# Optimization experiments

Measured on AMD Instinct MI355X. Metric: run time of the kernel, lower is better.

## Reference

```python
import jax, jax.numpy as jnp
import numpy as np

B, T, C = 2, 2048, 1024
H = 16
HS = C // H
EPS = 1e-5


def layernorm(x, g, b):
    mu = jnp.mean(x, axis=-1, keepdims=True)
    var = jnp.var(x, axis=-1, keepdims=True)
    return (x - mu) * jax.lax.rsqrt(var + EPS) * g + b


def setup_inputs() -> dict:
    key = jax.random.key(0)
    ks = jax.random.split(key, 12)
    s_in = 1.0 / np.sqrt(C)
    s_ff = 1.0 / np.sqrt(4 * C)
    return {
        "x": jax.random.normal(ks[0], (B, T, C), jnp.float32),
        "Wq": jax.random.normal(ks[1], (H, C, HS), jnp.float32) * s_in,
        "Wk": jax.random.normal(ks[2], (H, C, HS), jnp.float32) * s_in,
        "Wv": jax.random.normal(ks[3], (H, C, HS), jnp.float32) * s_in,
        "Wo": jax.random.normal(ks[4], (C, C), jnp.float32) * s_in,
        "bo": jnp.zeros((C,), jnp.float32),
        "W1": jax.random.normal(ks[5], (C, 4 * C), jnp.float32) * s_in,
        "b1": jnp.zeros((4 * C,), jnp.float32),
        "W2": jax.random.normal(ks[6], (4 * C, C), jnp.float32) * s_ff,
        "b2": jnp.zeros((C,), jnp.float32),
        "g1": jnp.ones((C,), jnp.float32),
        "be1": jnp.zeros((C,), jnp.float32),
        "g2": jnp.ones((C,), jnp.float32),
        "be2": jnp.zeros((C,), jnp.float32),
    }


def reference(x, Wq, Wk, Wv, Wo, bo, W1, b1, W2, b2, g1, be1, g2, be2):
    # x: [B,T,C]. Dropout is identity (eval mode).
    x = layernorm(x, g1, be1)
    # --- multi-head causal self-attention (per-source: scale by C**-0.5, NOT head_size) ---
    q = jnp.einsum("btc,hcd->bhtd", x, Wq)
    k = jnp.einsum("btc,hcd->bhtd", x, Wk)
    v = jnp.einsum("btc,hcd->bhtd", x, Wv)
    scores = jnp.einsum("bhtd,bhsd->bhts", q, k) * (C ** -0.5)  # [B,H,T,T]
    causal = jnp.tril(jnp.ones((T, T), bool))
    scores = jnp.where(causal, scores, -jnp.inf)
    wei = jax.nn.softmax(scores, axis=-1)
    attn = jnp.einsum("bhts,bhsd->bhtd", wei, v)
    attn = attn.transpose(0, 2, 1, 3).reshape(B, T, C)  # concat heads on last dim
    sa = attn @ Wo + bo
    x = x + sa
    # --- MLP with second pre-op LayerNorm ---
    x = layernorm(x, g2, be2)
    h = jax.nn.relu(x @ W1 + b1)
    x = x + (h @ W2 + b2)
    return x
```

## Files before the change

### kernel.cpp

```cpp
#include <hip/hip_runtime.h>
#include <hip/hip_bf16.h>
#include <math.h>

#define B_ 2
#define T_ 2048
#define C_ 1024
#define H_ 16
#define HS_ 64
#define N_ROWS (B_*T_)
#define MB (1024*1024)

typedef __attribute__((ext_vector_type(8))) short bf16x8;
typedef __attribute__((ext_vector_type(8))) unsigned short u16x8;
typedef __attribute__((ext_vector_type(4))) float floatx4;

static __device__ __forceinline__ unsigned short f2bf(float f) {
  union { float f; unsigned u; } v; v.f = f;
  unsigned r = v.u + 0x7fff + ((v.u >> 16) & 1);
  return (unsigned short)(r >> 16);
}
static __device__ __forceinline__ float bf2f(unsigned short s) {
  union { unsigned u; float f; } v; v.u = ((unsigned)s) << 16;
  return v.f;
}

__global__ __launch_bounds__(256) void ln_kernel(
    const float* __restrict__ x, const float* __restrict__ g,
    const float* __restrict__ b, unsigned short* __restrict__ outb)
{
  const int row = blockIdx.x;
  const int tid = threadIdx.x;
  const float* xr = x + (size_t)row * C_;
  float4 xv = *reinterpret_cast<const float4*>(xr + tid * 4);
  float s  = xv.x + xv.y + xv.z + xv.w;
  float ss = xv.x*xv.x + xv.y*xv.y + xv.z*xv.z + xv.w*xv.w;
  #pragma unroll
  for (int off = 32; off > 0; off >>= 1) {
    s  += __shfl_down(s, off, 64);
    ss += __shfl_down(ss, off, 64);
  }
  __shared__ float rs[4], rss[4];
  __shared__ float smu, srstd;
  if ((tid & 63) == 0) { rs[tid >> 6] = s; rss[tid >> 6] = ss; }
  __syncthreads();
  if (tid == 0) {
    float S  = rs[0] + rs[1] + rs[2] + rs[3];
    float SS = rss[0] + rss[1] + rss[2] + rss[3];
    float mu  = S * (1.0f / C_);
    float var = SS * (1.0f / C_) - mu * mu;
    smu = mu; srstd = rsqrtf(var + 1e-5f);
  }
  __syncthreads();
  const float mu = smu, rstd = srstd;
  float4 gv = *reinterpret_cast<const float4*>(g + tid * 4);
  float4 bv = *reinterpret_cast<const float4*>(b + tid * 4);
  union { unsigned long long ll; unsigned short s[4]; } o;
  o.s[0] = f2bf((xv.x - mu) * rstd * gv.x + bv.x);
  o.s[1] = f2bf((xv.y - mu) * rstd * gv.y + bv.y);
  o.s[2] = f2bf((xv.z - mu) * rstd * gv.z + bv.z);
  o.s[3] = f2bf((xv.w - mu) * rstd * gv.w + bv.w);
  *reinterpret_cast<unsigned long long*>(outb + (size_t)row * C_ + tid * 4) = o.ll;
}

__global__ __launch_bounds__(256) void transpose_cast(
    const float* __restrict__ in, unsigned short* __restrict__ out, int R, int Cc)
{
  __shared__ float tile[32][33];
  const int bz = blockIdx.z;
  in  += (size_t)bz * R * Cc;
  out += (size_t)bz * R * Cc;
  const int tx = threadIdx.x & 31;
  const int ty = threadIdx.x >> 5;
  const int c0 = blockIdx.x * 32, r0 = blockIdx.y * 32;
  #pragma unroll
  for (int j = 0; j < 4; ++j)
    tile[ty + j*8][tx] = in[(size_t)(r0 + ty + j*8) * Cc + c0 + tx];
  __syncthreads();
  #pragma unroll
  for (int j = 0; j < 4; ++j)
    out[(size_t)(c0 + ty + j*8) * R + r0 + tx] = f2bf(tile[tx][ty + j*8]);
}

__global__ __launch_bounds__(256) void transpose_cast_qkv(
    const float* __restrict__ Wq, const float* __restrict__ Wk,
    const float* __restrict__ Wv, unsigned short* __restrict__ out)
{
  __shared__ float tile[32][33];
  const int z = blockIdx.z;
  const int which = z >> 4, h = z & 15;
  const float* in = (which == 0 ? Wq : which == 1 ? Wk : Wv) + (size_t)h * C_ * HS_;
  unsigned short* dst = out + (size_t)z * C_ * HS_;
  const int tx = threadIdx.x & 31;
  const int ty = threadIdx.x >> 5;
  const int c0 = blockIdx.x * 32, r0 = blockIdx.y * 32;
  #pragma unroll
  for (int j = 0; j < 4; ++j)
    tile[ty + j*8][tx] = in[(size_t)(r0 + ty + j*8) * HS_ + c0 + tx];
  __syncthreads();
  #pragma unroll
  for (int j = 0; j < 4; ++j)
    dst[(size_t)(c0 + ty + j*8) * C_ + r0 + tx] = f2bf(tile[tx][ty + j*8]);
}

template<int TNB, bool OUTBF16, bool RELU, bool HASB, bool HASRES>
__global__ __launch_bounds__(256) void gemm_bf16(
    const unsigned short* __restrict__ A,
    const unsigned short* __restrict__ Bt,
    const float* __restrict__ bias,
    const unsigned short* __restrict__ res,
    void* __restrict__ Cout,
    int M, int N, int K)
{
  constexpr int NT = TNB / 32;
  constexpr int WN = TNB / 2;
  __shared__ unsigned short As[2][128 * 32];
  __shared__ unsigned short Bs[2][TNB * 32];
  const int tid  = threadIdx.x;
  const int lane = tid & 63;
  const int wave = tid >> 6;
  const int wm = wave & 1, wn = wave >> 1;
  const int m0 = blockIdx.x * 128, n0 = blockIdx.y * TNB;

  const int lrow = lane >> 2;
  const int lcol = (lane & 3) * 8;
  const int fr = lane & 15;
  const int fq = lane >> 4;

  floatx4 acc[4][NT] = {};

  const unsigned short* Aw = A  + (size_t)m0 * K;
  const unsigned short* Bw = Bt + (size_t)n0 * K;

  for (int k0 = 0; k0 < K; k0 += 64) {
    __syncthreads();
    #pragma unroll
    for (int half = 0; half < 2; ++half) {
      #pragma unroll
      for (int i = 0; i < 2; ++i) {
        const int rbase = i * 64 + wave * 16;
        const unsigned short* gp =
            Aw + (size_t)(rbase + lrow) * K + k0 + half * 32 + lcol;
        __builtin_amdgcn_global_load_lds(
            (const __attribute__((address_space(1))) void*)gp,
            (__attribute__((address_space(3))) void*)(As[half] + rbase * 32),
            16, 0, 0);
      }
      #pragma unroll
      for (int i = 0; i < TNB / 64; ++i) {
        const int rbase = i * 64 + wave * 16;
        const unsigned short* gp =
            Bw + (size_t)(rbase + lrow) * K + k0 + half * 32 + lcol;
        __builtin_amdgcn_global_load_lds(
            (const __attribute__((address_space(1))) void*)gp,
            (__attribute__((address_space(3))) void*)(Bs[half] + rbase * 32),
            16, 0, 0);
      }
    }
    __syncthreads();

    #pragma unroll
    for (int half = 0; half < 2; ++half) {
      bf16x8 af[4], bfr[NT];
      #pragma unroll
      for (int t = 0; t < 4; ++t)
        af[t]  = *reinterpret_cast<const bf16x8*>(
            As[half] + (wm*64 + t*16 + fr)*32 + fq*8);
      #pragma unroll
      for (int t = 0; t < NT; ++t)
        bfr[t] = *reinterpret_cast<const bf16x8*>(
            Bs[half] + (wn*WN + t*16 + fr)*32 + fq*8);
      #pragma unroll
      for (int mt = 0; mt < 4; ++mt)
        #pragma unroll
        for (int nt = 0; nt < NT; ++nt)
          acc[mt][nt] = __builtin_amdgcn_mfma_f32_16x16x32_bf16(
              af[mt], bfr[nt], acc[mt][nt], 0, 0, 0);
    }
  }

  #pragma unroll
  for (int nt = 0; nt < NT; ++nt) {
    const int col = n0 + wn*WN + nt*16 + fr;
    const float bv = HASB ? bias[col] : 0.0f;
    #pragma unroll
    for (int mt = 0; mt < 4; ++mt) {
      #pragma unroll
      for (int r = 0; r < 4; ++r) {
        const int row = m0 + wm*64 + mt*16 + fq*4 + r;
        float v = acc[mt][nt][r] + bv;
        if (RELU) v = v > 0.0f ? v : 0.0f;
        if (HASRES) v += bf2f(res[(size_t)row * N + col]);
        if (OUTBF16) ((unsigned short*)Cout)[(size_t)row * N + col] = f2bf(v);
        else         ((float*)Cout)[(size_t)row * N + col] = v;
      }
    }
  }
}

template<int TNB, int SPLITS>
__global__ __launch_bounds__(256) void gemm_splitk(
    const unsigned short* __restrict__ A,
    const unsigned short* __restrict__ Bt,
    unsigned short* __restrict__ Cpart,
    int M, int N, int Kfull)
{
  constexpr int NT = TNB / 32;
  constexpr int WN = TNB / 2;
  __shared__ unsigned short As[2][128 * 32];
  __shared__ unsigned short Bs[2][TNB * 32];
  const int tid  = threadIdx.x;
  const int lane = tid & 63;
  const int wave = tid >> 6;
  const int wm = wave & 1, wn = wave >> 1;
  const int m0 = blockIdx.x * 128, n0 = blockIdx.y * TNB;
  const int z  = blockIdx.z;
  const int Kh = Kfull / SPLITS;

  const int lrow = lane >> 2;
  const int lcol = (lane & 3) * 8;
  const int fr = lane & 15;
  const int fq = lane >> 4;

  floatx4 acc[4][NT] = {};

  const unsigned short* Aw = A  + (size_t)m0 * Kfull + (size_t)z * Kh;
  const unsigned short* Bw = Bt + (size_t)n0 * Kfull + (size_t)z * Kh;
  unsigned short* Cw = Cpart + (size_t)z * M * N;

  for (int k0 = 0; k0 < Kh; k0 += 64) {
    __syncthreads();
    #pragma unroll
    for (int half = 0; half < 2; ++half) {
      #pragma unroll
      for (int i = 0; i < 2; ++i) {
        const int rbase = i * 64 + wave * 16;
        const unsigned short* gp =
            Aw + (size_t)(rbase + lrow) * Kfull + k0 + half * 32 + lcol;
        __builtin_amdgcn_global_load_lds(
            (const __attribute__((address_space(1))) void*)gp,
            (__attribute__((address_space(3))) void*)(As[half] + rbase * 32),
            16, 0, 0);
      }
      #pragma unroll
      for (int i = 0; i < TNB / 64; ++i) {
        const int rbase = i * 64 + wave * 16;
        const unsigned short* gp =
            Bw + (size_t)(rbase + lrow) * Kfull + k0 + half * 32 + lcol;
        __builtin_amdgcn_global_load_lds(
            (const __attribute__((address_space(1))) void*)gp,
            (__attribute__((address_space(3))) void*)(Bs[half] + rbase * 32),
            16, 0, 0);
      }
    }
    __syncthreads();

    #pragma unroll
    for (int half = 0; half < 2; ++half) {
      bf16x8 af[4], bfr[NT];
      #pragma unroll
      for (int t = 0; t < 4; ++t)
        af[t]  = *reinterpret_cast<const bf16x8*>(
            As[half] + (wm*64 + t*16 + fr)*32 + fq*8);
      #pragma unroll
      for (int t = 0; t < NT; ++t)
        bfr[t] = *reinterpret_cast<const bf16x8*>(
            Bs[half] + (wn*WN + t*16 + fr)*32 + fq*8);
      #pragma unroll
      for (int mt = 0; mt < 4; ++mt)
        #pragma unroll
        for (int nt = 0; nt < NT; ++nt)
          acc[mt][nt] = __builtin_amdgcn_mfma_f32_16x16x32_bf16(
              af[mt], bfr[nt], acc[mt][nt], 0, 0, 0);
    }
  }

  #pragma unroll
  for (int nt = 0; nt < NT; ++nt) {
    const int col = n0 + wn*WN + nt*16 + fr;
    #pragma unroll
    for (int mt = 0; mt < 4; ++mt)
      #pragma unroll
      for (int r = 0; r < 4; ++r) {
        const int row = m0 + wm*64 + mt*16 + fq*4 + r;
        Cw[(size_t)row * N + col] = f2bf(acc[mt][nt][r]);
      }
  }
}

template<int SPLITS>
__global__ __launch_bounds__(256) void splitk_reduce(
    const unsigned short* __restrict__ p,
    const float* __restrict__ bias, const unsigned short* __restrict__ res,
    float* __restrict__ out)
{
  const size_t i = ((size_t)blockIdx.x * 256 + threadIdx.x) * 4;
  const size_t MN = (size_t)N_ROWS * C_;
  float4 bv = *reinterpret_cast<const float4*>(bias + (i & (size_t)(C_ - 1)));
  float acc[4] = {bv.x, bv.y, bv.z, bv.w};
  {
    const unsigned short* rp = res + i;
    #pragma unroll
    for (int j = 0; j < 4; ++j) acc[j] += bf2f(rp[j]);
  }
  #pragma unroll
  for (int z = 0; z < SPLITS; ++z) {
    const unsigned short* pp = p + (size_t)z * MN + i;
    #pragma unroll
    for (int j = 0; j < 4; ++j) acc[j] += bf2f(pp[j]);
  }
  float4 o; o.x = acc[0]; o.y = acc[1]; o.z = acc[2]; o.w = acc[3];
  *reinterpret_cast<float4*>(out + i) = o;
}

__global__ __launch_bounds__(256) void v_transpose(
    const unsigned short* __restrict__ qkv, unsigned short* __restrict__ vt)
{
  __shared__ __align__(16) unsigned short sT[64][72];
  const int st = blockIdx.x;
  const int bh = blockIdx.y;
  const int b = bh >> 4, h = bh & 15;
  const int t = threadIdx.x;
  const int r = t >> 2, c0 = (t & 3) * 16;
  const unsigned short* src =
      qkv + (size_t)(b * T_ + st * 64 + r) * 3072 + 2048 + h * 64 + c0;
  *(u16x8*)&sT[r][c0]     = *(const u16x8*)src;
  *(u16x8*)&sT[r][c0 + 8] = *(const u16x8*)(src + 8);
  __syncthreads();
  const int d = t >> 2, sc = (t & 3) * 16;
  unsigned short v[16];
  #pragma unroll
  for (int j = 0; j < 16; ++j) v[j] = sT[sc + j][d];
  unsigned short* dst = vt + ((size_t)bh * 64 + d) * (size_t)T_ + st * 64 + sc;
  *(uint4*)dst       = *(uint4*)&v[0];
  *(uint4*)(dst + 8) = *(uint4*)&v[8];
}

__global__ __launch_bounds__(256, 4) void attn_mfma(
    const unsigned short* __restrict__ qkv,
    const unsigned short* __restrict__ vt,
    unsigned short* __restrict__ out)
{
  const int bh = blockIdx.x;
  const int qt = (int)(gridDim.y - 1) - (int)blockIdx.y;
  const int b = bh >> 4, h = bh & 15;
  const int tid = threadIdx.x;
  const int w = tid >> 6;
  const int lane = tid & 63;
  const int l15 = lane & 15, fq = lane >> 4;
  const int t0 = qt * 64;
  const int q_row = t0 + w * 16 + l15;

  __shared__ __align__(16) unsigned short sK [64][72];
  __shared__ __align__(16) unsigned short sVt[64][72];
  __shared__ __align__(16) unsigned short sP [64][72];

  bf16x8 aq[2];
  {
    const unsigned short* qp = qkv + (size_t)(b*T_ + q_row)*3072 + h*HS_ + fq*8;
    aq[0] = *(const bf16x8*)qp;
    aq[1] = *(const bf16x8*)(qp + 32);
  }

  floatx4 oacc[4] = {};
  float m_s = -3.0e38f, l_s = 0.0f;
  const float c1 = 1.4426950408889634f / 32.0f;
  const int nks = qt + 1;

  for (int ks = 0; ks < nks; ++ks) {
    __syncthreads();
    {
      const int r = tid >> 2, c0 = (tid & 3) * 16;
      const unsigned short* kp =
          qkv + (size_t)(b*T_ + ks*64 + r)*3072 + C_ + h*HS_ + c0;
      u16x8 k0 = *(const u16x8*)kp, k1 = *(const u16x8*)(kp + 8);
      const unsigned short* vp =
          vt + ((size_t)bh*64 + r)*(size_t)T_ + ks*64 + c0;
      u16x8 v0 = *(const u16x8*)vp, v1 = *(const u16x8*)(vp + 8);
      *(u16x8*)&sK[r][c0]      = k0; *(u16x8*)&sK[r][c0 + 8]  = k1;
      *(u16x8*)&sVt[r][c0]     = v0; *(u16x8*)&sVt[r][c0 + 8] = v1;
    }
    __syncthreads();

    floatx4 stacc[4] = {};
    #pragma unroll
    for (int st = 0; st < 4; ++st) {
      bf16x8 k0 = *(const bf16x8*)&sK[st*16 + l15][fq*8];
      bf16x8 k1 = *(const bf16x8*)&sK[st*16 + l15][32 + fq*8];
      stacc[st] = __builtin_amdgcn_mfma_f32_16x16x32_bf16(k0, aq[0], stacc[st], 0, 0, 0);
      stacc[st] = __builtin_amdgcn_mfma_f32_16x16x32_bf16(k1, aq[1], stacc[st], 0, 0, 0);
    }

    if (ks == qt) {
      #pragma unroll
      for (int st = 0; st < 4; ++st)
        #pragma unroll
        for (int r = 0; r < 4; ++r) {
          const int s = ks*64 + st*16 + fq*4 + r;
          if (s > q_row) stacc[st][r] = -3.0e38f;
        }
    }

    float mx = -3.0e38f;
    #pragma unroll
    for (int st = 0; st < 4; ++st)
      #pragma unroll
      for (int r = 0; r < 4; ++r) mx = fmaxf(mx, stacc[st][r]);
    mx = fmaxf(mx, __shfl_xor(mx, 16, 64));
    mx = fmaxf(mx, __shfl_xor(mx, 32, 64));
    const float mnew = fmaxf(m_s, mx);
    const float alpha = exp2f((m_s - mnew) * c1);
    m_s = mnew;

    float sum = 0.0f;
    #pragma unroll
    for (int st = 0; st < 4; ++st) {
      unsigned pu[4];
      #pragma unroll
      for (int r = 0; r < 4; ++r) {
        const float p = exp2f((stacc[st][r] - mnew) * c1);
        sum += p;
        union { float f; unsigned u; } cv; cv.f = p;
        pu[r] = cv.u + 0x8000u;
      }
      const unsigned lo = __builtin_amdgcn_perm(pu[1], pu[0], 0x07060302u);
      const unsigned hi = __builtin_amdgcn_perm(pu[3], pu[2], 0x07060302u);
      const unsigned long long pk = ((unsigned long long)hi << 32) | lo;
      *(unsigned long long*)&sP[w*16 + l15][st*16 + fq*4] = pk;
    }
    sum += __shfl_xor(sum, 16, 64);
    sum += __shfl_xor(sum, 32, 64);
    l_s = l_s * alpha + sum;

    #pragma unroll
    for (int r = 0; r < 4; ++r) {
      const float ar = __shfl(alpha, fq*4 + r, 64);
      #pragma unroll
      for (int dt = 0; dt < 4; ++dt) oacc[dt][r] *= ar;
    }

    #pragma unroll
    for (int c = 0; c < 2; ++c) {
      bf16x8 ap = *(const bf16x8*)&sP[w*16 + l15][c*32 + fq*8];
      #pragma unroll
      for (int dt = 0; dt < 4; ++dt) {
        bf16x8 bv = *(const bf16x8*)&sVt[dt*16 + l15][c*32 + fq*8];
        oacc[dt] = __builtin_amdgcn_mfma_f32_16x16x32_bf16(ap, bv, oacc[dt], 0, 0, 0);
      }
    }
  }

  #pragma unroll
  for (int r = 0; r < 4; ++r) {
    const float il = 1.0f / __shfl(l_s, fq*4 + r, 64);
    const int q = t0 + w*16 + fq*4 + r;
    #pragma unroll
    for (int dt = 0; dt < 4; ++dt)
      out[(size_t)(b*T_ + q)*C_ + h*HS_ + dt*16 + l15] = f2bf(oacc[dt][r] * il);
  }
}

extern "C" void kernel_launch(void* const* d_in, const int* in_sizes, int n_in,
                              void* d_out, int out_size, void* d_ws, size_t ws_size,
                              hipStream_t stream)
{
  const float* x   = (const float*)d_in[0];
  const float* Wq  = (const float*)d_in[1];
  const float* Wk  = (const float*)d_in[2];
  const float* Wv  = (const float*)d_in[3];
  const float* Wo  = (const float*)d_in[4];
  const float* bo  = (const float*)d_in[5];
  const float* W1  = (const float*)d_in[6];
  const float* b1  = (const float*)d_in[7];
  const float* W2  = (const float*)d_in[8];
  const float* b2  = (const float*)d_in[9];
  const float* g1  = (const float*)d_in[10];
  const float* be1 = (const float*)d_in[11];
  const float* g2  = (const float*)d_in[12];
  const float* be2 = (const float*)d_in[13];
  float* out = (float*)d_out;

  char* ws = (char*)d_ws;
  unsigned short* BtQKV = (unsigned short*)(ws + (size_t) 0*MB);
  unsigned short* BtWo  = (unsigned short*)(ws + (size_t) 6*MB);
  unsigned short* BtW1  = (unsigned short*)(ws + (size_t) 8*MB);
  unsigned short* BtW2  = (unsigned short*)(ws + (size_t)16*MB);
  unsigned short* lnb   = (unsigned short*)(ws + (size_t)24*MB);
  unsigned short* qkvb  = (unsigned short*)(ws + (size_t)32*MB);
  unsigned short* vtb   = (unsigned short*)(ws + (size_t)56*MB);
  unsigned short* attnb = (unsigned short*)(ws + (size_t)64*MB);
  float*          x2    = (float*)         (ws + (size_t)32*MB);
  unsigned short* hb    = (unsigned short*)(ws + (size_t)32*MB);
  unsigned short* pk4   = (unsigned short*)(ws + (size_t)64*MB);

  dim3 blk(256);

  transpose_cast_qkv<<<dim3(HS_/32, C_/32, 3*H_), blk, 0, stream>>>(Wq, Wk, Wv, BtQKV);
  transpose_cast<<<dim3(C_/32,  C_/32, 1),  blk, 0, stream>>>(Wo, BtWo, C_, C_);
  transpose_cast<<<dim3(4*C_/32,C_/32, 1),  blk, 0, stream>>>(W1, BtW1, C_, 4*C_);
  transpose_cast<<<dim3(C_/32,4*C_/32, 1),  blk, 0, stream>>>(W2, BtW2, 4*C_, C_);

  ln_kernel<<<dim3(N_ROWS), blk, 0, stream>>>(x, g1, be1, lnb);

  gemm_bf16<128,true,false,false,false><<<dim3(N_ROWS/128, 3072/128), blk, 0, stream>>>(
      lnb, BtQKV, nullptr, nullptr, qkvb, N_ROWS, 3072, C_);

  v_transpose<<<dim3(T_/64, B_*H_), blk, 0, stream>>>(qkvb, vtb);

  attn_mfma<<<dim3(B_*H_, T_/64), blk, 0, stream>>>(qkvb, vtb, attnb);

  gemm_bf16<64,false,false,true,true><<<dim3(N_ROWS/128, C_/64), blk, 0, stream>>>(
      attnb, BtWo, bo, lnb, x2, N_ROWS, C_, C_);

  ln_kernel<<<dim3(N_ROWS), blk, 0, stream>>>(x2, g2, be2, lnb);

  gemm_bf16<128,true,true,true,false><<<dim3(N_ROWS/128, 4*C_/128), blk, 0, stream>>>(
      lnb, BtW1, b1, nullptr, hb, N_ROWS, 4*C_, C_);

  gemm_splitk<128,4><<<dim3(N_ROWS/128, C_/128, 4), blk, 0, stream>>>(
      hb, BtW2, pk4, N_ROWS, C_, 4*C_);

  splitk_reduce<4><<<dim3((N_ROWS * C_) / (256 * 4)), blk, 0, stream>>>(
      pk4, b2, lnb, out);
}
```

Before: 359.2 us.

## Pair causal query tiles per block and widen attention key tiles to 128

Each attention block now handles two query tiles (qt and 31-qt) in sequence, which balances causal work across blocks and halves the grid. Key/value tiles widen from 64 to 128 keys per iteration, which halves the number of barriers and loop trips. The online softmax gets a lazy rescale that skips the alpha correction when the running max grows by at most 8 in log2 units, and setprio hints wrap the MFMA sections. The risks are fewer blocks in flight, more LDS per block, and wasted masked work in the 128-key diagonal tile.

```diff
diff --git a/kernel.cpp b/kernel.cpp
--- a/kernel.cpp
+++ b/kernel.cpp
@@ -341,121 +341,146 @@
     unsigned short* __restrict__ out)
 {
   const int bh = blockIdx.x;
-  const int qt = (int)(gridDim.y - 1) - (int)blockIdx.y;
   const int b = bh >> 4, h = bh & 15;
   const int tid = threadIdx.x;
   const int w = tid >> 6;
   const int lane = tid & 63;
   const int l15 = lane & 15, fq = lane >> 4;
-  const int t0 = qt * 64;
-  const int q_row = t0 + w * 16 + l15;
-
-  __shared__ __align__(16) unsigned short sK [64][72];
-  __shared__ __align__(16) unsigned short sVt[64][72];
-  __shared__ __align__(16) unsigned short sP [64][72];
-
-  bf16x8 aq[2];
-  {
-    const unsigned short* qp = qkv + (size_t)(b*T_ + q_row)*3072 + h*HS_ + fq*8;
-    aq[0] = *(const bf16x8*)qp;
-    aq[1] = *(const bf16x8*)(qp + 32);
-  }
-
-  floatx4 oacc[4] = {};
-  float m_s = -3.0e38f, l_s = 0.0f;
+
+  __shared__ __align__(16) unsigned short sK [128][72];
+  __shared__ __align__(16) unsigned short sVt[64][136];
+  __shared__ __align__(16) unsigned short sP [64][136];
+
   const float c1 = 1.4426950408889634f / 32.0f;
-  const int nks = qt + 1;
-
-  for (int ks = 0; ks < nks; ++ks) {
-    __syncthreads();
+
+  #pragma unroll 1
+  for (int pass = 0; pass < 2; ++pass) {
+    const int qt = pass ? 31 - (int)blockIdx.y : (int)blockIdx.y;
+    const int t0 = qt * 64;
+    const int q_row = t0 + w * 16 + l15;
+
+    bf16x8 aq[2];
     {
-      const int r = tid >> 2, c0 = (tid & 3) * 16;
-      const unsigned short* kp =
-          qkv + (size_t)(b*T_ + ks*64 + r)*3072 + C_ + h*HS_ + c0;
-      u16x8 k0 = *(const u16x8*)kp, k1 = *(const u16x8*)(kp + 8);
-      const unsigned short* vp =
-          vt + ((size_t)bh*64 + r)*(size_t)T_ + ks*64 + c0;
-      u16x8 v0 = *(const u16x8*)vp, v1 = *(const u16x8*)(vp + 8);
-      *(u16x8*)&sK[r][c0]      = k0; *(u16x8*)&sK[r][c0 + 8]  = k1;
-      *(u16x8*)&sVt[r][c0]     = v0; *(u16x8*)&sVt[r][c0 + 8] = v1;
-    }
-    __syncthreads();
-
-    floatx4 stacc[4] = {};
-    #pragma unroll
-    for (int st = 0; st < 4; ++st) {
-      bf16x8 k0 = *(const bf16x8*)&sK[st*16 + l15][fq*8];
-      bf16x8 k1 = *(const bf16x8*)&sK[st*16 + l15][32 + fq*8];
-      stacc[st] = __builtin_amdgcn_mfma_f32_16x16x32_bf16(k0, aq[0], stacc[st], 0, 0, 0);
-      stacc[st] = __builtin_amdgcn_mfma_f32_16x16x32_bf16(k1, aq[1], stacc[st], 0, 0, 0);
-    }
-
-    if (ks == qt) {
-      #pragma unroll
-      for (int st = 0; st < 4; ++st)
+      const unsigned short* qp = qkv + (size_t)(b*T_ + q_row)*3072 + h*HS_ + fq*8;
+      aq[0] = *(const bf16x8*)qp;
+      aq[1] = *(const bf16x8*)(qp + 32);
+    }
+
+    floatx4 oacc[4] = {};
+    float m_s = -3.0e38f, l_s = 0.0f;
+    const int nks = (qt >> 1) + 1;
+
+    #pragma unroll 1
+    for (int ks = 0; ks < nks; ++ks) {
+      __syncthreads();
+      {
+        const int r  = tid >> 1, c0 = (tid & 1) * 32;
+        const unsigned short* kp =
+            qkv + (size_t)(b*T_ + ks*128 + r)*3072 + C_ + h*HS_ + c0;
+        u16x8 k0 = *(const u16x8*)kp;
+        u16x8 k1 = *(const u16x8*)(kp + 8);
+        u16x8 k2 = *(const u16x8*)(kp + 16);
+        u16x8 k3 = *(const u16x8*)(kp + 24);
+        const int r2 = tid >> 2, c2 = (tid & 3) * 32;
+        const unsigned short* vp =
+            vt + ((size_t)bh*64 + r2)*(size_t)T_ + ks*128 + c2;
+        u16x8 v0 = *(const u16x8*)vp;
+        u16x8 v1 = *(const u16x8*)(vp + 8);
+        u16x8 v2 = *(const u16x8*)(vp + 16);
+        u16x8 v3 = *(const u16x8*)(vp + 24);
+        *(u16x8*)&sK[r][c0]        = k0; *(u16x8*)&sK[r][c0 + 8]   = k1;
+        *(u16x8*)&sK[r][c0 + 16]   = k2; *(u16x8*)&sK[r][c0 + 24]  = k3;
+        *(u16x8*)&sVt[r2][c2]      = v0; *(u16x8*)&sVt[r2][c2 + 8] = v1;
+        *(u16x8*)&sVt[r2][c2 + 16] = v2; *(u16x8*)&sVt[r2][c2 + 24] = v3;
+      }
+      __syncthreads();
+
+      floatx4 stacc[8] = {};
+      __builtin_amdgcn_s_setprio(1);
+      #pragma unroll
+      for (int st = 0; st < 8; ++st) {
+        bf16x8 k0 = *(const bf16x8*)&sK[st*16 + l15][fq*8];
+        bf16x8 k1 = *(const bf16x8*)&sK[st*16 + l15][32 + fq*8];
+        stacc[st] = __builtin_amdgcn_mfma_f32_16x16x32_bf16(k0, aq[0], stacc[st], 0, 0, 0);
+        stacc[st] = __builtin_amdgcn_mfma_f32_16x16x32_bf16(k1, aq[1], stacc[st], 0, 0, 0);
+      }
+      __builtin_amdgcn_s_setprio(0);
+
+      if (ks == nks - 1) {
+        const int sbase = ks*128 + fq*4;
+        #pragma unroll
+        for (int st = 0; st < 8; ++st)
+          #pragma unroll
+          for (int r = 0; r < 4; ++r)
+            if (sbase + st*16 + r > q_row) stacc[st][r] = -3.0e38f;
+      }
+
+      float mx = -3.0e38f;
+      #pragma unroll
+      for (int st = 0; st < 8; ++st)
+        #pragma unroll
+        for (int r = 0; r < 4; ++r) mx = fmaxf(mx, stacc[st][r]);
+      mx = fmaxf(mx, __shfl_xor(mx, 16, 64));
+      mx = fmaxf(mx, __shfl_xor(mx, 32, 64));
+
+      float mnew;
+      if (__all((mx - m_s) * c1 <= 8.0f)) {
+        mnew = m_s;
+      } else {
+        mnew = fmaxf(m_s, mx);
+        const float alpha = exp2f((m_s - mnew) * c1);
         #pragma unroll
         for (int r = 0; r < 4; ++r) {
-          const int s = ks*64 + st*16 + fq*4 + r;
-          if (s > q_row) stacc[st][r] = -3.0e38f;
+          const float ar = __shfl(alpha, fq*4 + r, 64);
+          #pragma unroll
+          for (int dt = 0; dt < 4; ++dt) oacc[dt][r] *= ar;
         }
-    }
-
-    float mx = -3.0e38f;
-    #pragma unroll
-    for (int st = 0; st < 4; ++st)
-      #pragma unroll
-      for (int r = 0; r < 4; ++r) mx = fmaxf(mx, stacc[st][r]);
-    mx = fmaxf(mx, __shfl_xor(mx, 16, 64));
-    mx = fmaxf(mx, __shfl_xor(mx, 32, 64));
-    const float mnew = fmaxf(m_s, mx);
-    const float alpha = exp2f((m_s - mnew) * c1);
-    m_s = mnew;
-
-    float sum = 0.0f;
-    #pragma unroll
-    for (int st = 0; st < 4; ++st) {
-      unsigned pu[4];
-      #pragma unroll
-      for (int r = 0; r < 4; ++r) {
-        const float p = exp2f((stacc[st][r] - mnew) * c1);
-        sum += p;
-        union { float f; unsigned u; } cv; cv.f = p;
-        pu[r] = cv.u + 0x8000u;
-      }
-      const unsigned lo = __builtin_amdgcn_perm(pu[1], pu[0], 0x07060302u);
-      const unsigned hi = __builtin_amdgcn_perm(pu[3], pu[2], 0x07060302u);
-      const unsigned long long pk = ((unsigned long long)hi << 32) | lo;
-      *(unsigned long long*)&sP[w*16 + l15][st*16 + fq*4] = pk;
-    }
-    sum += __shfl_xor(sum, 16, 64);
-    sum += __shfl_xor(sum, 32, 64);
-    l_s = l_s * alpha + sum;
+        l_s *= alpha;
+        m_s = mnew;
+      }
+
+      const float mc = mnew * c1;
+      float sum = 0.0f;
+      #pragma unroll
+      for (int st = 0; st < 8; ++st) {
+        unsigned pu[4];
+        #pragma unroll
+        for (int r = 0; r < 4; ++r) {
+          const float p = exp2f(stacc[st][r] * c1 - mc);
+          sum += p;
+          union { float f; unsigned u; } cv; cv.f = p;
+          pu[r] = cv.u + 0x8000u;
+        }
+        const unsigned lo = __builtin_amdgcn_perm(pu[1], pu[0], 0x07060302u);
+        const unsigned hi = __builtin_amdgcn_perm(pu[3], pu[2], 0x07060302u);
+        *(unsigned long long*)&sP[w*16 + l15][st*16 + fq*4] =
+            ((unsigned long long)hi << 32) | lo;
+      }
+      sum += __shfl_xor(sum, 16, 64);
+      sum += __shfl_xor(sum, 32, 64);
+      l_s += sum;
+
+      __builtin_amdgcn_s_setprio(1);
+      #pragma unroll
+      for (int c = 0; c < 4; ++c) {
+        bf16x8 ap = *(const bf16x8*)&sP[w*16 + l15][c*32 + fq*8];
+        #pragma unroll
+        for (int dt = 0; dt < 4; ++dt) {
+          bf16x8 bv = *(const bf16x8*)&sVt[dt*16 + l15][c*32 + fq*8];
+          oacc[dt] = __builtin_amdgcn_mfma_f32_16x16x32_bf16(ap, bv, oacc[dt], 0, 0, 0);
+        }
+      }
+      __builtin_amdgcn_s_setprio(0);
+    }
 
     #pragma unroll
     for (int r = 0; r < 4; ++r) {
-      const float ar = __shfl(alpha, fq*4 + r, 64);
-      #pragma unroll
-      for (int dt = 0; dt < 4; ++dt) oacc[dt][r] *= ar;
-    }
-
-    #pragma unroll
-    for (int c = 0; c < 2; ++c) {
-      bf16x8 ap = *(const bf16x8*)&sP[w*16 + l15][c*32 + fq*8];
-      #pragma unroll
-      for (int dt = 0; dt < 4; ++dt) {
-        bf16x8 bv = *(const bf16x8*)&sVt[dt*16 + l15][c*32 + fq*8];
-        oacc[dt] = __builtin_amdgcn_mfma_f32_16x16x32_bf16(ap, bv, oacc[dt], 0, 0, 0);
-      }
-    }
-  }
-
-  #pragma unroll
-  for (int r = 0; r < 4; ++r) {
-    const float il = 1.0f / __shfl(l_s, fq*4 + r, 64);
-    const int q = t0 + w*16 + fq*4 + r;
-    #pragma unroll
-    for (int dt = 0; dt < 4; ++dt)
-      out[(size_t)(b*T_ + q)*C_ + h*HS_ + dt*16 + l15] = f2bf(oacc[dt][r] * il);
+      const float il = 1.0f / __shfl(l_s, fq*4 + r, 64);
+      const int q = t0 + w*16 + fq*4 + r;
+      #pragma unroll
+      for (int dt = 0; dt < 4; ++dt)
+        out[(size_t)(b*T_ + q)*C_ + h*HS_ + dt*16 + l15] = f2bf(oacc[dt][r] * il);
+    }
   }
 }
 
@@ -506,7 +531,7 @@
 
   v_transpose<<<dim3(T_/64, B_*H_), blk, 0, stream>>>(qkvb, vtb);
 
-  attn_mfma<<<dim3(B_*H_, T_/64), blk, 0, stream>>>(qkvb, vtb, attnb);
+  attn_mfma<<<dim3(B_*H_, T_/128), blk, 0, stream>>>(qkvb, vtb, attnb);
 
   gemm_bf16<64,false,false,true,true><<<dim3(N_ROWS/128, C_/64), blk, 0, stream>>>(
       attnb, BtWo, bo, lnb, x2, N_ROWS, C_, C_);
```

Result: no change. 358.1 us (-0.3%).
